# Performance work log

Hardware: AMD Instinct MI355X
Metric: run time of the kernel (lower is better)

Reference implementation:

```python
import jax, jax.numpy as jnp
import numpy as np

M, K, L, D_OUT = 8, 12, 9, 32           # ferns, bits/fern, patch size, vote dim
N, C, H, W = 64, 8, 128, 128            # batch, channels, image size
HP, WP = H - L + 1, W - L + 1           # valid word-map size (120, 120)
POOL = 7                                # AvgPool2d kernel, stride 1
TEMP = 0.1                              # soft-bit annealing temperature


def setup_inputs() -> dict:
    key = jax.random.key(0)
    ks = jax.random.split(key, 5)
    x = jax.random.normal(ks[0], (N, C, H, W), dtype=jnp.float32)
    thresholds = jax.random.normal(ks[1], (M, K), dtype=jnp.float32) * 0.1
    table = jax.random.normal(ks[2], (M, 2 ** K, D_OUT), dtype=jnp.float32) * 0.05
    chan_idx = jax.random.randint(ks[3], (M, K, 2), 0, C, dtype=jnp.int32)
    offsets = jax.random.randint(ks[4], (M, K, 2, 2), 0, L, dtype=jnp.int32)
    return dict(x=x, thresholds=thresholds, table=table,
                chan_idx=chan_idx, offsets=offsets)


def _shifted_plane(x, c, dy, dx):
    # x: (N,C,H,W) -> (N,HP,WP) pixel plane at channel c shifted by (dy,dx)
    return jax.lax.dynamic_slice(x, (0, c, dy, dx), (N, 1, HP, WP))[:, 0]


def reference(x, thresholds, table, chan_idx, offsets):
    # --- FernBitWord: K thresholded pixel-pair differences per fern ---
    def bit_fn(c2, off2):
        p1 = _shifted_plane(x, c2[0], off2[0, 0], off2[0, 1])
        p2 = _shifted_plane(x, c2[1], off2[1, 0], off2[1, 1])
        return p1 - p2                                   # (N,HP,WP)

    flat_c = chan_idx.reshape(M * K, 2)
    flat_o = offsets.reshape(M * K, 2, 2)
    diff = jax.vmap(bit_fn)(flat_c, flat_o).reshape(M, K, N, HP, WP)

    s = jax.nn.sigmoid((diff - thresholds[:, :, None, None, None]) / TEMP)
    bits = s > 0.5                                       # hard bit values
    pow2 = (2 ** jnp.arange(K, dtype=jnp.int32))[None, :, None, None, None]
    words = jnp.sum(bits.astype(jnp.int32) * pow2, axis=1)   # (M,N,HP,WP)
    conf = jnp.prod(jnp.where(bits, s, 1.0 - s), axis=1)     # (M,N,HP,WP)

    # --- FernSparseTable: per-fern voting-table lookup, accumulated over ferns ---
    def step(acc, mkw):
        tbl_m, w_m, c_m = mkw
        return acc + tbl_m[w_m] * c_m[..., None], None   # (N,HP,WP,D)

    init = jnp.zeros((N, HP, WP, D_OUT), dtype=x.dtype)
    votes, _ = jax.lax.scan(step, init, (table, words, conf))
    votes = jnp.transpose(votes, (0, 3, 1, 2))           # (N,D,HP,WP)

    # --- AvgPool2d(kernel=POOL, stride=1) + flatten ---
    pooled = jax.lax.reduce_window(
        votes, 0.0, jax.lax.add, (1, 1, POOL, POOL), (1, 1, 1, 1), 'VALID'
    ) / (POOL * POOL)
    return pooled.reshape(N, -1)
```

## Files before the change

### kernel.cpp

```cpp
#include <hip/hip_runtime.h>
#include <hip/hip_fp16.h>


#define NN 64
#define CC 8
#define HH 128
#define WW 128
#define MM 8
#define KK 12
#define DD 32
#define OUTS 114
#define TT 19
#define PT 25
#define XT 33
#define XSTRIDE (XT*XT)
#define VSTRIDE 36
#define NPOSI (PT*PT)
#define THREADS 640
#define POOLW 7

#define PTK 24
#define XTK 32
#define NPOS_IMG (120*120)
#define K1_THREADS (PTK*PTK)

#define WC_PLANE ((size_t)NN * NPOS_IMG * 16)
#define WC_BYTES (3 * WC_PLANE)

#define LDS_BYTES (CC*XSTRIDE*4 + NPOSI*VSTRIDE*2)

__device__ __forceinline__ float4 ld4h(const __half* p) {
    union { float2 f; __half2 h[2]; } u;
    u.f = *(const float2*)p;
    float2 a = __half22float2(u.h[0]);
    float2 b = __half22float2(u.h[1]);
    return make_float4(a.x, a.y, b.x, b.y);
}
__device__ __forceinline__ void st4h(__half* p, float4 v) {
    union { float2 f; __half2 h[2]; } u;
    u.h[0] = __floats2half2_rn(v.x, v.y);
    u.h[1] = __floats2half2_rn(v.z, v.w);
    *(float2*)p = u.f;
}

template<int XS, int XROW>
__device__ __forceinline__ void fern_bits(const float* __restrict__ xs, int pb,
                                          const float* __restrict__ thresholds,
                                          const int*   __restrict__ chan_idx,
                                          const int*   __restrict__ offsets,
                                          unsigned wreg[MM], float creg[MM])
{
    #pragma unroll
    for (int m = 0; m < MM; ++m) {
        unsigned word = 0u;
        float P = 1.f;
        #pragma unroll
        for (int k = 0; k < KK; ++k) {
            const int mk = m*KK + k;
            int c1  = chan_idx[mk*2 + 0];
            int c2  = chan_idx[mk*2 + 1];
            int dy1 = offsets[mk*4 + 0];
            int dx1 = offsets[mk*4 + 1];
            int dy2 = offsets[mk*4 + 2];
            int dx2 = offsets[mk*4 + 3];
            float thr = thresholds[mk];
            float p1 = xs[c1*XS + dy1*XROW + dx1 + pb];
            float p2 = xs[c2*XS + dy2*XROW + dx2 + pb];
            float z  = (p1 - p2) - thr;
            if (z > 0.f) word |= (1u << k);
            float e = __expf(-10.f * fabsf(z));
            P += P * e;
        }
        wreg[m] = word;
        creg[m] = __builtin_amdgcn_rcpf(P);
    }
}

__global__ __launch_bounds__(K1_THREADS, 8)
void fern_words(const float* __restrict__ x,
                const float* __restrict__ thresholds,
                const int*   __restrict__ chan_idx,
                const int*   __restrict__ offsets,
                uint4*  __restrict__ wq,
                float4* __restrict__ cq0,
                float4* __restrict__ cq1)
{
    __shared__ float4 xs4[CC*XTK*XTK/4];
    float* xs = (float*)xs4;

    const int tile = blockIdx.x;
    const int n    = tile / 25;
    const int t2   = tile - n*25;
    const int pi0  = (t2 / 5) * PTK;
    const int pj0  = (t2 % 5) * PTK;

    const int tid = threadIdx.x;

    const float* xn = x + (size_t)n * (CC*HH*WW);
    for (int idx = tid; idx < CC*XTK*XTK/4; idx += K1_THREADS) {
        int c   = idx >> 8;
        int rem = idx & 255;
        int r   = rem >> 3;
        int c4  = rem & 7;
        xs4[idx] = *(const float4*)(xn + (c*HH + pi0 + r)*WW + pj0 + c4*4);
    }
    __syncthreads();

    const int ty = tid / PTK;
    const int tx = tid - ty*PTK;
    const int pb = ty*XTK + tx;

    unsigned wreg[MM];
    float    creg[MM];
    fern_bits<CC*XTK*XTK/CC == 1024 ? 1024 : 1024, XTK>(xs, pb, thresholds,
                                                        chan_idx, offsets,
                                                        wreg, creg);

    const int gp = n*NPOS_IMG + (pi0 + ty)*120 + (pj0 + tx);
    uint4 wv;
    wv.x = wreg[0] | (wreg[1] << 16);
    wv.y = wreg[2] | (wreg[3] << 16);
    wv.z = wreg[4] | (wreg[5] << 16);
    wv.w = wreg[6] | (wreg[7] << 16);
    wq[gp]  = wv;
    cq0[gp] = make_float4(creg[0], creg[1], creg[2], creg[3]);
    cq1[gp] = make_float4(creg[4], creg[5], creg[6], creg[7]);
}

__global__ __launch_bounds__(THREADS, 8)
void fern_votes(const float* __restrict__ table,
                const uint4*  __restrict__ wq,
                const float4* __restrict__ cq0,
                const float4* __restrict__ cq1,
                float* __restrict__ out)
{
    __shared__ float2 vsraw[NPOSI*VSTRIDE/4];
    __half* vs = (__half*)vsraw;

    const int tile = blockIdx.x;
    const int n    = tile / 36;
    const int t2   = tile - n*36;
    const int ti   = t2 / 6;
    const int tj   = t2 - ti*6;
    const int i0   = ti * TT;
    const int j0   = tj * TT;

    const int tid = threadIdx.x;

    const int pbase = n*NPOS_IMG + i0*120 + j0;
    for (int item = tid; item < NPOSI*8; item += THREADS) {
        const int pos = item >> 3;
        const int d4  = item & 7;
        const int y   = pos / PT;
        const int j   = pos - y*PT;
        const int gp  = pbase + y*120 + j;
        uint4  wv = wq[gp];
        float4 c0 = cq0[gp];
        float4 c1 = cq1[gp];
        const float* tb = table + d4*4;
        float4 acc = make_float4(0.f, 0.f, 0.f, 0.f);
        unsigned w; float cf; float4 tv;
#define FERN(mi, wexpr, cexpr)                                             \
        w = (wexpr); cf = (cexpr);                                         \
        tv = *(const float4*)(tb + ((size_t)(mi) << 17) + w*DD);           \
        acc.x += cf*tv.x; acc.y += cf*tv.y;                                \
        acc.z += cf*tv.z; acc.w += cf*tv.w;
        FERN(0, wv.x & 0xFFFFu, c0.x)
        FERN(1, wv.x >> 16,     c0.y)
        FERN(2, wv.y & 0xFFFFu, c0.z)
        FERN(3, wv.y >> 16,     c0.w)
        FERN(4, wv.z & 0xFFFFu, c1.x)
        FERN(5, wv.z >> 16,     c1.y)
        FERN(6, wv.w & 0xFFFFu, c1.z)
        FERN(7, wv.w >> 16,     c1.w)
#undef FERN
        st4h(vs + pos*VSTRIDE + d4*4, acc);
    }
    __syncthreads();

    for (int w = tid; w < PT*8; w += THREADS) {
        int y  = w / 8;
        int d4 = w - y*8;
        float4 s = make_float4(0.f, 0.f, 0.f, 0.f);
        float4 ring[POOLW];
        #pragma unroll
        for (int j = 0; j < PT; ++j) {
            float4 v = ld4h(vs + (y*PT + j)*VSTRIDE + d4*4);
            if (j >= POOLW) {
                float4 o = ring[j % POOLW];
                s.x -= o.x; s.y -= o.y; s.z -= o.z; s.w -= o.w;
            }
            ring[j % POOLW] = v;
            s.x += v.x; s.y += v.y; s.z += v.z; s.w += v.w;
            if (j >= POOLW-1)
                st4h(vs + (y*PT + (j - POOLW + 1))*VSTRIDE + d4*4, s);
        }
    }
    __syncthreads();

    const float inv = 1.f / 49.f;
    float* outn = out + (size_t)n * (DD*OUTS*OUTS);
    for (int w = tid; w < 8*TT; w += THREADS) {
        int d4 = w / TT;
        int jo = w - d4*TT;
        float4 s = make_float4(0.f, 0.f, 0.f, 0.f);
        float4 ring[POOLW];
        #pragma unroll
        for (int y = 0; y < PT; ++y) {
            float4 v = ld4h(vs + (y*PT + jo)*VSTRIDE + d4*4);
            if (y >= POOLW) {
                float4 o = ring[y % POOLW];
                s.x -= o.x; s.y -= o.y; s.z -= o.z; s.w -= o.w;
            }
            ring[y % POOLW] = v;
            s.x += v.x; s.y += v.y; s.z += v.z; s.w += v.w;
            if (y >= POOLW-1) {
                int io = y - POOLW + 1;
                size_t base = ((size_t)(d4*4)*OUTS + (i0 + io))*OUTS + (j0 + jo);
                outn[base                      ] = s.x * inv;
                outn[base +   (size_t)OUTS*OUTS] = s.y * inv;
                outn[base + 2*(size_t)OUTS*OUTS] = s.z * inv;
                outn[base + 3*(size_t)OUTS*OUTS] = s.w * inv;
            }
        }
    }
}

__global__ __launch_bounds__(THREADS, 5)
void fern_fused(const float* __restrict__ x,
                const float* __restrict__ thresholds,
                const float* __restrict__ table,
                const int*   __restrict__ chan_idx,
                const int*   __restrict__ offsets,
                float* __restrict__ out)
{
    extern __shared__ float smem[];
    float*  xs = smem;
    __half* vs = (__half*)(smem + CC*XSTRIDE);

    const int tile = blockIdx.x;
    const int n    = tile / 36;
    const int t2   = tile - n*36;
    const int ti   = t2 / 6;
    const int tj   = t2 - ti*6;
    const int i0   = ti * TT;
    const int j0   = tj * TT;
    const int tid = threadIdx.x;

    const float* xn = x + (size_t)n * (CC*HH*WW);
    for (int idx = tid; idx < CC*XSTRIDE; idx += THREADS) {
        int c   = idx / XSTRIDE;
        int rem = idx - c*XSTRIDE;
        int r   = rem / XT;
        int col = rem - r*XT;
        xs[idx] = xn[(c*HH + (i0 + r))*WW + (j0 + col)];
    }
    __syncthreads();

    unsigned wreg[MM];
    float    creg[MM];
    if (tid < NPOSI) {
        const int y  = tid / PT;
        const int j  = tid - y*PT;
        fern_bits<XSTRIDE, XT>(xs, y*XT + j, thresholds, chan_idx, offsets,
                               wreg, creg);
    }
    __syncthreads();

    float* cbuf = smem;
    uint4* wbuf = (uint4*)(smem + 5000);

    if (tid < NPOSI) {
        uint4 wv;
        wv.x = wreg[0] | (wreg[1] << 16);
        wv.y = wreg[2] | (wreg[3] << 16);
        wv.z = wreg[4] | (wreg[5] << 16);
        wv.w = wreg[6] | (wreg[7] << 16);
        wbuf[tid] = wv;
        ((float4*)cbuf)[tid*2 + 0] = make_float4(creg[0], creg[1], creg[2], creg[3]);
        ((float4*)cbuf)[tid*2 + 1] = make_float4(creg[4], creg[5], creg[6], creg[7]);
    }
    __syncthreads();

    for (int item = tid; item < NPOSI*8; item += THREADS) {
        const int pos = item >> 3;
        const int d4  = item & 7;
        uint4  wv = wbuf[pos];
        float4 c0 = ((const float4*)cbuf)[pos*2 + 0];
        float4 c1 = ((const float4*)cbuf)[pos*2 + 1];
        const float* tb = table + d4*4;
        float4 acc = make_float4(0.f, 0.f, 0.f, 0.f);
        unsigned w; float cf; float4 tv;
#define FERN(mi, wexpr, cexpr)                                             \
        w = (wexpr); cf = (cexpr);                                         \
        tv = *(const float4*)(tb + ((size_t)(mi) << 17) + w*DD);           \
        acc.x += cf*tv.x; acc.y += cf*tv.y;                                \
        acc.z += cf*tv.z; acc.w += cf*tv.w;
        FERN(0, wv.x & 0xFFFFu, c0.x)
        FERN(1, wv.x >> 16,     c0.y)
        FERN(2, wv.y & 0xFFFFu, c0.z)
        FERN(3, wv.y >> 16,     c0.w)
        FERN(4, wv.z & 0xFFFFu, c1.x)
        FERN(5, wv.z >> 16,     c1.y)
        FERN(6, wv.w & 0xFFFFu, c1.z)
        FERN(7, wv.w >> 16,     c1.w)
#undef FERN
        st4h(vs + pos*VSTRIDE + d4*4, acc);
    }
    __syncthreads();

    for (int w = tid; w < PT*8; w += THREADS) {
        int y  = w / 8;
        int d4 = w - y*8;
        float4 s = make_float4(0.f, 0.f, 0.f, 0.f);
        float4 ring[POOLW];
        #pragma unroll
        for (int j = 0; j < PT; ++j) {
            float4 v = ld4h(vs + (y*PT + j)*VSTRIDE + d4*4);
            if (j >= POOLW) {
                float4 o = ring[j % POOLW];
                s.x -= o.x; s.y -= o.y; s.z -= o.z; s.w -= o.w;
            }
            ring[j % POOLW] = v;
            s.x += v.x; s.y += v.y; s.z += v.z; s.w += v.w;
            if (j >= POOLW-1)
                st4h(vs + (y*PT + (j - POOLW + 1))*VSTRIDE + d4*4, s);
        }
    }
    __syncthreads();

    const float inv = 1.f / 49.f;
    float* outn = out + (size_t)n * (DD*OUTS*OUTS);
    for (int w = tid; w < 8*TT; w += THREADS) {
        int d4 = w / TT;
        int jo = w - d4*TT;
        float4 s = make_float4(0.f, 0.f, 0.f, 0.f);
        float4 ring[POOLW];
        #pragma unroll
        for (int y = 0; y < PT; ++y) {
            float4 v = ld4h(vs + (y*PT + jo)*VSTRIDE + d4*4);
            if (y >= POOLW) {
                float4 o = ring[y % POOLW];
                s.x -= o.x; s.y -= o.y; s.z -= o.z; s.w -= o.w;
            }
            ring[y % POOLW] = v;
            s.x += v.x; s.y += v.y; s.z += v.z; s.w += v.w;
            if (y >= POOLW-1) {
                int io = y - POOLW + 1;
                size_t base = ((size_t)(d4*4)*OUTS + (i0 + io))*OUTS + (j0 + jo);
                outn[base                      ] = s.x * inv;
                outn[base +   (size_t)OUTS*OUTS] = s.y * inv;
                outn[base + 2*(size_t)OUTS*OUTS] = s.z * inv;
                outn[base + 3*(size_t)OUTS*OUTS] = s.w * inv;
            }
        }
    }
}

extern "C" void kernel_launch(void* const* d_in, const int* in_sizes, int n_in,
                              void* d_out, int out_size, void* d_ws, size_t ws_size,
                              hipStream_t stream) {
    const float* x          = (const float*)d_in[0];
    const float* thresholds = (const float*)d_in[1];
    const float* table      = (const float*)d_in[2];
    const int*   chan_idx   = (const int*)d_in[3];
    const int*   offsets    = (const int*)d_in[4];
    float* out = (float*)d_out;

    if (d_ws != nullptr && ws_size >= WC_BYTES) {
        char*   wsb = (char*)d_ws;
        uint4*  wq  = (uint4*)wsb;
        float4* cq0 = (float4*)(wsb + WC_PLANE);
        float4* cq1 = (float4*)(wsb + 2*WC_PLANE);
        fern_words<<<dim3(NN*25), dim3(K1_THREADS), 0, stream>>>(
            x, thresholds, chan_idx, offsets, wq, cq0, cq1);
        fern_votes<<<dim3(NN*36), dim3(THREADS), 0, stream>>>(
            table, wq, cq0, cq1, out);
    } else {
        hipFuncSetAttribute((const void*)fern_fused,
                            hipFuncAttributeMaxDynamicSharedMemorySize, LDS_BYTES);
        fern_fused<<<dim3(NN*36), dim3(THREADS), LDS_BYTES, stream>>>(
            x, thresholds, table, chan_idx, offsets, out);
    }
}
```

Baseline: 332.2 us.

## Move table gather into word kernel and pass fp16 votes to pool kernel

Restructures the two-kernel split. The first kernel now computes the fern words and confidences, stages them in LDS, does the table gather per position, and writes fp16 vote vectors to workspace. The second kernel only loads those votes and runs the average pool. This removes the halo recompute of gathers in overlapping pool tiles and the word/confidence round trip. In exchange the intermediate traffic changes from 48 bytes to 64 bytes per position, and the gather now runs inside a kernel with a smaller block.

```diff
diff --git a/kernel.cpp b/kernel.cpp
--- a/kernel.cpp
+++ b/kernel.cpp
@@ -24,8 +24,7 @@
 #define NPOS_IMG (120*120)
 #define K1_THREADS (PTK*PTK)
 
-#define WC_PLANE ((size_t)NN * NPOS_IMG * 16)
-#define WC_BYTES (3 * WC_PLANE)
+#define VOTE_BYTES ((size_t)NN * NPOS_IMG * DD * 2)
 
 #define LDS_BYTES (CC*XSTRIDE*4 + NPOSI*VSTRIDE*2)
 
@@ -77,13 +76,12 @@
 }
 
 __global__ __launch_bounds__(K1_THREADS, 8)
-void fern_words(const float* __restrict__ x,
-                const float* __restrict__ thresholds,
-                const int*   __restrict__ chan_idx,
-                const int*   __restrict__ offsets,
-                uint4*  __restrict__ wq,
-                float4* __restrict__ cq0,
-                float4* __restrict__ cq1)
+void fern_gather(const float* __restrict__ x,
+                 const float* __restrict__ thresholds,
+                 const float* __restrict__ table,
+                 const int*   __restrict__ chan_idx,
+                 const int*   __restrict__ offsets,
+                 __half* __restrict__ votes)
 {
     __shared__ float4 xs4[CC*XTK*XTK/4];
     float* xs = (float*)xs4;
@@ -108,55 +106,36 @@
 
     const int ty = tid / PTK;
     const int tx = tid - ty*PTK;
-    const int pb = ty*XTK + tx;
 
     unsigned wreg[MM];
     float    creg[MM];
-    fern_bits<CC*XTK*XTK/CC == 1024 ? 1024 : 1024, XTK>(xs, pb, thresholds,
-                                                        chan_idx, offsets,
-                                                        wreg, creg);
-
-    const int gp = n*NPOS_IMG + (pi0 + ty)*120 + (pj0 + tx);
-    uint4 wv;
-    wv.x = wreg[0] | (wreg[1] << 16);
-    wv.y = wreg[2] | (wreg[3] << 16);
-    wv.z = wreg[4] | (wreg[5] << 16);
-    wv.w = wreg[6] | (wreg[7] << 16);
-    wq[gp]  = wv;
-    cq0[gp] = make_float4(creg[0], creg[1], creg[2], creg[3]);
-    cq1[gp] = make_float4(creg[4], creg[5], creg[6], creg[7]);
-}
-
-__global__ __launch_bounds__(THREADS, 8)
-void fern_votes(const float* __restrict__ table,
-                const uint4*  __restrict__ wq,
-                const float4* __restrict__ cq0,
-                const float4* __restrict__ cq1,
-                float* __restrict__ out)
-{
-    __shared__ float2 vsraw[NPOSI*VSTRIDE/4];
-    __half* vs = (__half*)vsraw;
-
-    const int tile = blockIdx.x;
-    const int n    = tile / 36;
-    const int t2   = tile - n*36;
-    const int ti   = t2 / 6;
-    const int tj   = t2 - ti*6;
-    const int i0   = ti * TT;
-    const int j0   = tj * TT;
-
-    const int tid = threadIdx.x;
-
-    const int pbase = n*NPOS_IMG + i0*120 + j0;
-    for (int item = tid; item < NPOSI*8; item += THREADS) {
-        const int pos = item >> 3;
-        const int d4  = item & 7;
-        const int y   = pos / PT;
-        const int j   = pos - y*PT;
-        const int gp  = pbase + y*120 + j;
-        uint4  wv = wq[gp];
-        float4 c0 = cq0[gp];
-        float4 c1 = cq1[gp];
+    fern_bits<XTK*XTK, XTK>(xs, ty*XTK + tx, thresholds, chan_idx, offsets,
+                            wreg, creg);
+    __syncthreads();
+
+    float4* cbuf = (float4*)xs;
+    uint4*  wbuf = (uint4*)(xs + 4608);
+
+    {
+        uint4 wv;
+        wv.x = wreg[0] | (wreg[1] << 16);
+        wv.y = wreg[2] | (wreg[3] << 16);
+        wv.z = wreg[4] | (wreg[5] << 16);
+        wv.w = wreg[6] | (wreg[7] << 16);
+        wbuf[tid] = wv;
+        cbuf[tid*2 + 0] = make_float4(creg[0], creg[1], creg[2], creg[3]);
+        cbuf[tid*2 + 1] = make_float4(creg[4], creg[5], creg[6], creg[7]);
+    }
+    __syncthreads();
+
+    #pragma unroll
+    for (int it = 0; it < 8; ++it) {
+        const int item = tid + it*K1_THREADS;
+        const int pos  = item >> 3;
+        const int d4   = item & 7;
+        uint4  wv = wbuf[pos];
+        float4 c0 = cbuf[pos*2 + 0];
+        float4 c1 = cbuf[pos*2 + 1];
         const float* tb = table + d4*4;
         float4 acc = make_float4(0.f, 0.f, 0.f, 0.f);
         unsigned w; float cf; float4 tv;
@@ -174,7 +153,41 @@
         FERN(6, wv.w & 0xFFFFu, c1.z)
         FERN(7, wv.w >> 16,     c1.w)
 #undef FERN
-        st4h(vs + pos*VSTRIDE + d4*4, acc);
+        const int py = pos / PTK;
+        const int px = pos - py*PTK;
+        const int gp = n*NPOS_IMG + (pi0 + py)*120 + (pj0 + px);
+        union { float2 f; __half2 h[2]; } u;
+        u.h[0] = __floats2half2_rn(acc.x, acc.y);
+        u.h[1] = __floats2half2_rn(acc.z, acc.w);
+        *(float2*)(votes + (size_t)gp*DD + d4*4) = u.f;
+    }
+}
+
+__global__ __launch_bounds__(THREADS, 8)
+void fern_pool(const __half* __restrict__ votes,
+               float* __restrict__ out)
+{
+    __shared__ float2 vsraw[NPOSI*VSTRIDE/4];
+    __half* vs = (__half*)vsraw;
+
+    const int tile = blockIdx.x;
+    const int n    = tile / 36;
+    const int t2   = tile - n*36;
+    const int ti   = t2 / 6;
+    const int tj   = t2 - ti*6;
+    const int i0   = ti * TT;
+    const int j0   = tj * TT;
+
+    const int tid = threadIdx.x;
+
+    const int pbase = n*NPOS_IMG + i0*120 + j0;
+    for (int idx = tid; idx < NPOSI*8; idx += THREADS) {
+        const int pos = idx >> 3;
+        const int oct = idx & 7;
+        const int y   = pos / PT;
+        const int j   = pos - y*PT;
+        const __half* src = votes + (size_t)(pbase + y*120 + j)*DD + oct*4;
+        *(float2*)(vs + pos*VSTRIDE + oct*4) = *(const float2*)src;
     }
     __syncthreads();
 
@@ -367,15 +380,11 @@
     const int*   offsets    = (const int*)d_in[4];
     float* out = (float*)d_out;
 
-    if (d_ws != nullptr && ws_size >= WC_BYTES) {
-        char*   wsb = (char*)d_ws;
-        uint4*  wq  = (uint4*)wsb;
-        float4* cq0 = (float4*)(wsb + WC_PLANE);
-        float4* cq1 = (float4*)(wsb + 2*WC_PLANE);
-        fern_words<<<dim3(NN*25), dim3(K1_THREADS), 0, stream>>>(
-            x, thresholds, chan_idx, offsets, wq, cq0, cq1);
-        fern_votes<<<dim3(NN*36), dim3(THREADS), 0, stream>>>(
-            table, wq, cq0, cq1, out);
+    if (d_ws != nullptr && ws_size >= VOTE_BYTES) {
+        __half* votes = (__half*)d_ws;
+        fern_gather<<<dim3(NN*25), dim3(K1_THREADS), 0, stream>>>(
+            x, thresholds, table, chan_idx, offsets, votes);
+        fern_pool<<<dim3(NN*36), dim3(THREADS), 0, stream>>>(votes, out);
     } else {
         hipFuncSetAttribute((const void*)fern_fused,
                             hipFuncAttributeMaxDynamicSharedMemorySize, LDS_BYTES);
```

Result: no change. 335.1 us (+0.9%).
